# Kernel tuning notes

Hardware: AMD Instinct MI355X
Metric: run time of the kernel (lower is better)

The kernel has to match this reference:

```python
import jax, jax.numpy as jnp
import numpy as np

B, F, HU, HC = 8192, 100, 128, 512


def _lin(key, din, dout, bias=True, scale=0.02):
    k1, k2 = jax.random.split(key)
    w = jax.random.normal(k1, (din, dout), jnp.float32) * scale
    if bias:
        b = jax.random.normal(k2, (dout,), jnp.float32) * scale
        return w, b
    return (w,)


def setup_inputs() -> dict:
    key = jax.random.key(0)
    ks = jax.random.split(key, 24)
    d = {}
    d['feature_list'] = jax.random.normal(ks[0], (B, F), jnp.float32)
    d['is_treat'] = jax.random.uniform(ks[1], (B,), jnp.float32)
    d['emb'] = jax.random.normal(ks[2], (F, HU), jnp.float32) * 0.02
    d['t_w'], d['t_b'] = _lin(ks[3], 1, HU)
    d['qw'], d['qb'] = _lin(ks[4], HU, HU)
    d['kw'], d['kb'] = _lin(ks[5], HU, HU)
    d['vw'], d['vb'] = _lin(ks[6], HU, HU)
    (d['a1w'],) = _lin(ks[7], HU, HU, bias=False)
    d['a2w'], d['a2b'] = _lin(ks[8], HU, HU)
    (d['a3w'],) = _lin(ks[9], HU, 1, bias=False)
    d['c1w'], d['c1b'] = _lin(ks[10], F * HU, HC)
    d['c2w'], d['c2b'] = _lin(ks[11], HC, HC)
    d['c3w'], d['c3b'] = _lin(ks[12], HC, HC // 2)
    d['c4w'], d['c4b'] = _lin(ks[13], HC // 2, HC // 4)
    d['c5w'], d['c5b'] = _lin(ks[14], HC // 4, HC // 8)
    d['clw'], d['clb'] = _lin(ks[15], HC // 8, 1)
    d['ctw'], d['ctb'] = _lin(ks[16], HC // 8, 1)
    d['u1w'], d['u1b'] = _lin(ks[17], HU, HU)
    d['u2w'], d['u2b'] = _lin(ks[18], HU, HU // 2)
    d['u3w'], d['u3b'] = _lin(ks[19], HU // 2, HU // 4)
    d['u4w'], d['u4b'] = _lin(ks[20], HU // 4, HU // 8)
    d['tlw'], d['tlb'] = _lin(ks[21], HU // 8, 1)
    d['utw'], d['utb'] = _lin(ks[22], HU // 8, 1)
    return d


def reference(feature_list, is_treat, emb, t_w, t_b, qw, qb, kw, kb, vw, vb,
              a1w, a2w, a2b, a3w, c1w, c1b, c2w, c2b, c3w, c3b, c4w, c4b,
              c5w, c5b, clw, clb, ctw, ctb, u1w, u1b, u2w, u2b, u3w, u3b,
              u4w, u4b, tlw, tlb, utw, utb):
    elu = jax.nn.elu
    sig = jax.nn.sigmoid
    b, f = feature_list.shape
    h = emb.shape[1]
    # per-feature embedding: [B, F, H]
    x_rep = feature_list[:, :, None] * emb[None, :, :]
    # normalize over the feature axis (dim=1), as in torch.linalg.norm(dim=1)
    nx = x_rep / jnp.linalg.norm(x_rep, axis=1, keepdims=True)
    # self-attention with sigmoid-then-softmax scores
    Q = nx @ qw + qb
    K = nx @ kw + kb
    V = nx @ vw + vb
    scores = jnp.einsum('bfh,bgh->bfg', Q, K) / (h ** 0.5)
    attn_w = jax.nn.softmax(sig(scores), axis=-1)
    xx = jnp.einsum('bfg,bgh->bfh', attn_w, V).reshape(b, f * h)
    # control net tower
    c = elu(xx @ c1w + c1b)
    c = elu(c @ c2w + c2b)
    c = elu(c @ c3w + c3b)
    c = elu(c @ c4w + c4b)
    c = elu(c @ c5w + c5b)  # is_self=True
    c_logit = c @ clw + clb
    c_tau = c @ ctw + ctb
    c_prob = sig(c_logit)
    # treatment representation: Linear(1, hu) on ones -> [B, H]
    t_rep = jnp.ones((b, 1), feature_list.dtype) @ t_w.reshape(1, h) + t_b
    # interaction attention (vectorized over features)
    att = jax.nn.relu(sig(t_rep @ a1w)[:, None, :] + sig(x_rep @ a2w + a2b))
    att = (att @ a3w)[..., 0]  # [B, F]
    attn = jax.nn.softmax(att, axis=1)
    xt = jnp.einsum('bf,bfh->bh', attn, x_rep)
    # uplift net tower
    u = elu(xt @ u1w + u1b)
    u = elu(u @ u2w + u2b)
    u = elu(u @ u3w + u3b)
    u = elu(u @ u4w + u4b)  # is_self=True
    t_logit = u @ tlw + tlb
    u_tau = u @ utw + utb
    t_prob = sig(t_logit)
    return (c_logit, c_prob, c_tau, t_logit, t_prob, u_tau)
```

## Files before the change

kernel.cpp:

```cpp
#include <hip/hip_runtime.h>
#include <hip/hip_bf16.h>

typedef __bf16 bf16;
typedef __bf16 bf16x8 __attribute__((ext_vector_type(8)));
typedef __bf16 bf16x4 __attribute__((ext_vector_type(4)));
typedef float f32x4 __attribute__((ext_vector_type(4)));
typedef unsigned u32x4 __attribute__((ext_vector_type(4)));

#define DEVI static __device__ __forceinline__

DEVI float sigmoidf_(float x){ return 1.0f/(1.0f+__expf(-x)); }
DEVI float eluf_(float x){ return x>0.f ? x : (__expf(x)-1.f); }
DEVI f32x4 mfma16(bf16x8 a, bf16x8 b, f32x4 c){ return __builtin_amdgcn_mfma_f32_16x16x32_bf16(a,b,c,0,0,0); }
DEVI f32x4 mfma8(long a, long b, f32x4 c){ return __builtin_amdgcn_mfma_f32_16x16x32_fp8_fp8(a,b,c,0,0,0); }
DEVI unsigned pack2_(float a, float b){
    union { bf16 v[2]; unsigned u; } t; t.v[0]=(bf16)a; t.v[1]=(bf16)b; return t.u;
}
DEVI unsigned long long pack4_(float a, float b, float c, float d){
    union { bf16 v[4]; unsigned long long u; } t;
    t.v[0]=(bf16)a; t.v[1]=(bf16)b; t.v[2]=(bf16)c; t.v[3]=(bf16)d; return t.u;
}
DEVI unsigned cvtfp8x4_(float a, float b, float c, float d){
    int v = __builtin_amdgcn_cvt_pk_fp8_f32(a, b, 0, false);
    v = __builtin_amdgcn_cvt_pk_fp8_f32(c, d, v, true);
    return (unsigned)v;
}

#define B_ 8192
#define F_ 100
#define FP 112
#define H_ 128
#define KC_ 12800
#define SPLIT_ 4
#define FP8SC 16.0f

#define SWZ(r,bc) ((bc) ^ (((r)&7)<<4))

DEVI void dotrans_(float (*t)[33], const float* in, bf16* out, int R, int C, int bx, int by, int tid){
    int c0 = bx*32, r0 = by*32;
    int tc = tid & 31, tr = tid >> 5;
    #pragma unroll
    for (int i=0;i<4;i++){
        int r = tr + i*8;
        t[r][tc] = in[(size_t)(r0+r)*C + c0 + tc];
    }
    __syncthreads();
    #pragma unroll
    for (int i=0;i<4;i++){
        int ro = tr + i*8;
        out[(size_t)(c0+ro)*R + r0 + tc] = (bf16)t[tc][ro];
    }
}

__global__ void k_prep_all(const float* __restrict__ qw, const float* __restrict__ qb,
                           const float* __restrict__ kw, const float* __restrict__ kb,
                           const float* __restrict__ tw, const float* __restrict__ tb,
                           const float* __restrict__ a1w, const float* __restrict__ vw,
                           const float* __restrict__ a2w, const float* __restrict__ c2w,
                           const float* __restrict__ c3w,
                           bf16* __restrict__ mextT, float* __restrict__ sigt, float* __restrict__ cconst,
                           bf16* __restrict__ wvT, bf16* __restrict__ wa2t,
                           bf16* __restrict__ c2wt, bf16* __restrict__ c3wt){
    __shared__ float t[32][33];
    const float rsc = 0.08838834764831845f;
    int blk = blockIdx.x, tid = threadIdx.x;
    if (blk < 9){
        #pragma unroll 1
        for (int e=0; e<8; ++e){
            int idx = e*256 + tid;
            int n = blk*16 + (idx>>7), h = idx&127;
            float acc = 0.f;
            if (n < 128){
                for (int d=0; d<128; ++d) acc += qw[h*128+d]*kw[n*128+d];
            } else if (n == 128){
                for (int d=0; d<128; ++d) acc += qw[h*128+d]*kb[d];
            } else if (n == 129){
                for (int d=0; d<128; ++d) acc += kw[h*128+d]*qb[d];
            }
            mextT[n*128+h] = (bf16)(acc*rsc);
        }
    } else if (blk == 9){
        if (tid < 128){
            float acc = 0.f;
            for (int h=0; h<128; ++h) acc += (tw[h]+tb[h]) * a1w[h*128+tid];
            sigt[tid] = sigmoidf_(acc);
        } else if (tid == 128){
            float acc = 0.f;
            for (int d=0; d<128; ++d) acc += qb[d]*kb[d];
            cconst[0] = acc*rsc;
        }
    } else if (blk < 26){
        int i = blk-10; dotrans_(t, vw, wvT, 128,128, i&3, i>>2, tid);
    } else if (blk < 42){
        int i = blk-26; dotrans_(t, a2w, wa2t, 128,128, i&3, i>>2, tid);
    } else if (blk < 298){
        int i = blk-42; dotrans_(t, c2w, c2wt, 512,512, i&15, i>>4, tid);
    } else {
        int i = blk-298; dotrans_(t, c3w, c3wt, 512,256, i&7, i>>3, tid);
    }
}

DEVI int kappa_(int k){
    int f = k>>7, h = k&127;
    if (f < 96)
        return (((f>>4)<<3) | (h>>4))*256 + ((f&15)>>2)*64 + (h&15)*4 + (f&3);
    else
        return 12288 + (h>>4)*64 + (h&15)*4 + (f&3);
}

__global__ __launch_bounds__(256,2) void k_gk(
    const float* __restrict__ c1w, unsigned char* __restrict__ c1wtk8,
    const float* __restrict__ feat, const float* __restrict__ emb,
    const bf16* __restrict__ wa2t, const float* __restrict__ a2b,
    const float* __restrict__ a3w, const float* __restrict__ sigt,
    float* __restrict__ attg)
{
    __shared__ char A[37888];
    int blk = blockIdx.x, tid = threadIdx.x;
    if (blk < 6400){
        float (*t)[33] = (float(*)[33])A;
        const int C = 512;
        int c0 = (blk&15)*32, r0 = (blk>>4)*32;
        int tc = tid & 31, tr = tid >> 5;
        #pragma unroll
        for (int i=0;i<4;i++){
            int r = tr + i*8;
            t[r][tc] = c1w[(size_t)(r0+r)*C + c0 + tc];
        }
        __syncthreads();
        #pragma unroll
        for (int i=0;i<4;i++){
            int ro = tr + i*8;
            float x = t[tc][ro]*FP8SC;
            int v = __builtin_amdgcn_cvt_pk_fp8_f32(x, x, 0, false);
            c1wtk8[(size_t)(c0+ro)*KC_ + kappa_(r0+tc)] = (unsigned char)v;
        }
        return;
    }
    bf16 (*sAt)[72] = (bf16(*)[72])A;
    bf16 (*sBt)[72] = (bf16(*)[72])(A + 18432);
    float (*sRed)[128] = (float(*)[128])(A + 36864);
    int w=tid>>6, lane=tid&63, l15=lane&15, l4=lane>>4;
    int m0 = (blk-6400)*128;
    int wr = w>>1, wc = w&1;
    f32x4 acc[4][4];
    #pragma unroll
    for(int mi=0;mi<4;mi++)
        #pragma unroll
        for(int ni=0;ni<4;ni++) acc[mi][ni] = (f32x4){0.f,0.f,0.f,0.f};

    #pragma unroll 1
    for (int k0=0; k0<128; k0+=64){
        __syncthreads();
        #pragma unroll
        for (int t4=0; t4<4; t4++){
            int t = tid + t4*256;
            int row=t>>3, col=(t&7)*8;
            int gr = m0+row;
            int bb = gr/112, ff = gr - bb*112;
            bf16x8 o;
            if (ff < F_){
                float fv = feat[(size_t)bb*F_ + ff];
                const float* ep = emb + ff*H_ + k0 + col;
                f32x4 e0 = *(const f32x4*)ep;
                f32x4 e1 = *(const f32x4*)(ep+4);
                o[0]=(bf16)(fv*e0[0]); o[1]=(bf16)(fv*e0[1]); o[2]=(bf16)(fv*e0[2]); o[3]=(bf16)(fv*e0[3]);
                o[4]=(bf16)(fv*e1[0]); o[5]=(bf16)(fv*e1[1]); o[6]=(bf16)(fv*e1[2]); o[7]=(bf16)(fv*e1[3]);
            } else {
                #pragma unroll
                for (int e=0;e<8;e++) o[e]=(bf16)0.f;
            }
            *(bf16x8*)&sAt[row][col] = o;
            *(bf16x8*)&sBt[row][col] = *(const bf16x8*)(wa2t + row*H_ + k0 + col);
        }
        __syncthreads();
        #pragma unroll
        for(int ks=0;ks<2;ks++){
            bf16x8 af[4], bfr[4];
            #pragma unroll
            for(int mi=0;mi<4;mi++) af[mi] = *(const bf16x8*)&sAt[wr*64+mi*16+l15][ks*32+l4*8];
            #pragma unroll
            for(int ni=0;ni<4;ni++) bfr[ni] = *(const bf16x8*)&sBt[wc*64+ni*16+l15][ks*32+l4*8];
            #pragma unroll
            for(int mi=0;mi<4;mi++)
                #pragma unroll
                for(int ni=0;ni<4;ni++)
                    acc[mi][ni] = mfma16(af[mi], bfr[ni], acc[mi][ni]);
        }
    }
    float sg[4], ab[4], a3[4];
    #pragma unroll
    for (int ni=0;ni<4;ni++){
        int n = wc*64 + ni*16 + l15;
        sg[ni]=sigt[n]; ab[ni]=a2b[n]; a3[ni]=a3w[n];
    }
    #pragma unroll
    for (int mi=0;mi<4;mi++){
        float sj[4] = {0.f,0.f,0.f,0.f};
        #pragma unroll
        for (int ni=0;ni<4;ni++){
            #pragma unroll
            for (int j=0;j<4;j++){
                float u = sigmoidf_(acc[mi][ni][j] + ab[ni]);
                float t = sg[ni] + u;
                t = t>0.f ? t : 0.f;
                sj[j] += t*a3[ni];
            }
        }
        #pragma unroll
        for (int j=0;j<4;j++){
            float v = sj[j];
            #pragma unroll
            for (int m=1;m<16;m<<=1) v += __shfl_xor(v,m,16);
            sj[j]=v;
        }
        if (l15==0){
            #pragma unroll
            for (int j=0;j<4;j++) sRed[wc][wr*64+mi*16+l4*4+j] = sj[j];
        }
    }
    __syncthreads();
    if (tid < 128) attg[(size_t)m0 + tid] = sRed[0][tid] + sRed[1][tid];
}

__global__ __launch_bounds__(512,2) void k_attn2(
    const float* __restrict__ feat, const float* __restrict__ emb,
    const bf16* __restrict__ mextT, const bf16* __restrict__ wvT,
    const float* __restrict__ vb, const float* __restrict__ cconst,
    const float* __restrict__ attg,
    unsigned char* __restrict__ xxb, bf16* __restrict__ xtb)
{
    __shared__ char L[81792];
    char* Lm = L;
    char* Ln = L + 32768;
    float* sFeat  = (float*)(L+61440);
    float* normP  = (float*)(L+62336);
    float* sAw    = (float*)(L+77568);
    float* sNorm  = (float*)(L+79872);
    float* sAlpha = (float*)(L+80384);
    float* sBeta  = (float*)(L+80832);
    float* sInv   = (float*)(L+81280);

    int b = blockIdx.x;
    int tid = threadIdx.x, w = tid>>6, lane = tid&63;
    int l15 = lane&15, l4 = lane>>4;
    bf16 (*sP)[72] = (bf16(*)[72])(L + 61440 + w*2304);

    bf16x8 awv[4];
    #pragma unroll
    for (int kc=0;kc<4;kc++)
        awv[kc] = *(const bf16x8*)(wvT + (w*16+l15)*H_ + kc*32 + l4*8);
    float vbr = vb[w*16+l15];

    #pragma unroll 2
    for (int v = tid; v < 128*16; v += 512){
        int n = v >> 4, cg = (v & 15) * 8;
        *(u32x4*)(Lm + n*256 + SWZ(n, cg*2)) = *(const u32x4*)(mextT + n*128 + cg);
    }
    if (tid < FP) sFeat[tid] = (tid<F_) ? feat[(size_t)b*F_+tid] : 0.f;
    if (w==0){
        const float* ag = attg + (size_t)b*FP;
        float a0 = (lane<F_)? ag[lane] : -1e30f;
        float a1 = (lane+64<F_)? ag[lane+64] : -1e30f;
        float m = fmaxf(a0,a1);
        #pragma unroll
        for(int s=1;s<64;s<<=1) m = fmaxf(m, __shfl_xor(m,s,64));
        float e0 = (lane<F_)? __expf(a0-m):0.f;
        float e1 = (lane+64<F_)? __expf(a1-m):0.f;
        float s = e0+e1;
        #pragma unroll
        for(int t=1;t<64;t<<=1) s += __shfl_xor(s,t,64);
        float inv = 1.f/s;
        if (lane<FP) sAw[lane] = e0*inv;
        if (lane+64<FP) sAw[lane+64] = e1*inv;
    }
    __syncthreads();

    int hp = (tid&63)*2, gg = tid>>6;
    {
        float fa0=0.f, fa1=0.f;
        #pragma unroll 4
        for (int it=0; it<13; ++it){
            int f = gg + 8*it;
            if (f < F_){
                float2 e2 = *(const float2*)(emb + f*H_ + hp);
                float v0 = sFeat[f]*e2.x, v1 = sFeat[f]*e2.y;
                fa0 += v0*v0; fa1 += v1*v1;
            }
        }
        *(float2*)(normP + gg*128 + hp) = make_float2(fa0, fa1);
    }
    __syncthreads();
    if (tid < 128){
        float s = 0.f;
        #pragma unroll
        for (int g2=0; g2<8; ++g2) s += normP[g2*128 + tid];
        sNorm[tid] = sqrtf(s);
    }
    __syncthreads();

    {
        float rn0 = __builtin_amdgcn_rcpf(sNorm[hp]);
        float rn1 = __builtin_amdgcn_rcpf(sNorm[hp+1]);
        #pragma unroll 4
        for (int it=0; it<13; ++it){
            int f = gg + 8*it;
            if (f < F_){
                float2 e2 = *(const float2*)(emb + f*H_ + hp);
                *(unsigned*)(Ln + f*256 + SWZ(f, hp*2)) = pack2_(sFeat[f]*e2.x*rn0, sFeat[f]*e2.y*rn1);
            }
        }
        for (int z=tid; z<768; z+=512){
            int f = 100 + (z>>6), hz = (z&63)*2;
            *(unsigned*)(Ln + f*256 + SWZ(f, hz*2)) = 0u;
        }
    }
    __syncthreads();

    int mt = w;

    if (mt < 7){
        bf16x8 bfr8[4];
        #pragma unroll
        for (int kc=0;kc<4;kc++)
            bfr8[kc] = *(const bf16x8*)(mextT + (128+(l15&1))*H_ + kc*32 + l4*8);
        f32x4 acc = {0.f,0.f,0.f,0.f};
        #pragma unroll
        for (int kc=0;kc<4;kc++){
            bf16x8 a = *(const bf16x8*)(Ln + (mt*16+l15)*256 + SWZ(mt*16+l15, (kc*32+l4*8)*2));
            acc = mfma16(a, bfr8[kc], acc);
        }
        if (l15==0){
            #pragma unroll
            for (int j=0;j<4;j++) sAlpha[mt*16+l4*4+j] = acc[j];
        }
        if (l15==1){
            #pragma unroll
            for (int j=0;j<4;j++) sBeta[mt*16+l4*4+j] = acc[j];
        }
    }
    __syncthreads();

    const float cc = cconst[0];
    unsigned long long uexB[3];
    if (mt < 7){
        bf16x8 afxi[4];
        #pragma unroll
        for (int kc=0;kc<4;kc++)
            afxi[kc] = *(const bf16x8*)(Ln + (mt*16+l15)*256 + SWZ(mt*16+l15, (kc*32+l4*8)*2));
        f32x4 sc[7];
        #pragma unroll
        for (int gt=0; gt<7; gt++) sc[gt] = (f32x4){0.f,0.f,0.f,0.f};
        #pragma unroll
        for (int p=0; p<2; p++){
            #pragma unroll
            for (int nt4=0; nt4<4; nt4++){
                int nt = p*4 + nt4;
                bf16x8 bw[4];
                #pragma unroll
                for (int kc=0;kc<4;kc++)
                    bw[kc] = *(const bf16x8*)(Lm + (nt*16+l15)*256 + SWZ(nt*16+l15, (kc*32+l4*8)*2));
                f32x4 d = {0.f,0.f,0.f,0.f};
                #pragma unroll
                for (int kc=0;kc<4;kc++) d = mfma16(bw[kc], afxi[kc], d);
                *(unsigned long long*)(&sP[l15][nt4*16 + l4*4]) = pack4_(d[0],d[1],d[2],d[3]);
            }
            bf16x8 afs0 = *(const bf16x8*)&sP[l15][l4*8];
            bf16x8 afs1 = *(const bf16x8*)&sP[l15][32+l4*8];
            #pragma unroll
            for (int gt=0; gt<7; gt++){
                int r = gt*16+l15;
                bf16x8 b0 = *(const bf16x8*)(Ln + r*256 + SWZ(r, (p*64 + l4*8)*2));
                bf16x8 b1 = *(const bf16x8*)(Ln + r*256 + SWZ(r, (p*64 + 32 + l4*8)*2));
                sc[gt] = mfma16(b0, afs0, sc[gt]);
                sc[gt] = mfma16(b1, afs1, sc[gt]);
            }
        }
        float aj = sAlpha[mt*16+l15];
        float rs = 0.f;
        #pragma unroll
        for (int gt=0; gt<7; gt++){
            f32x4 bt4 = *(const f32x4*)&sBeta[gt*16+l4*4];
            float e[4];
            #pragma unroll
            for (int j=0;j<4;j++){
                int g = gt*16 + l4*4 + j;
                float val = sc[gt][j] + aj + bt4[j] + cc;
                e[j] = (g<F_) ? __expf(sigmoidf_(val)) : 0.f;
                rs += e[j];
            }
            if (gt < 4)
                *(unsigned long long*)(&sP[l15][gt*16 + l4*4]) = pack4_(e[0],e[1],e[2],e[3]);
            else
                uexB[gt-4] = pack4_(e[0],e[1],e[2],e[3]);
        }
        rs += __shfl_xor(rs, 16, 64);
        rs += __shfl_xor(rs, 32, 64);
        if (l4 == 0) sInv[w*16 + l15] = 1.f/rs;
    } else {
        int h = lane;
        float a0=0.f, a1=0.f;
        #pragma unroll 4
        for (int f=0; f<F_; ++f){
            float awf = sAw[f];
            a0 += awf * (float)*(const bf16*)(Ln + f*256 + SWZ(f, h*2));
            a1 += awf * (float)*(const bf16*)(Ln + f*256 + SWZ(f, (h+64)*2));
        }
        xtb[(size_t)b*H_ + h]      = (bf16)(a0 * sNorm[h]);
        xtb[(size_t)b*H_ + h + 64] = (bf16)(a1 * sNorm[h+64]);
    }

    unsigned long long vpku[7];
    #pragma unroll
    for (int gt=0; gt<7; gt++){
        f32x4 acc = {0.f,0.f,0.f,0.f};
        #pragma unroll
        for (int kc=0;kc<4;kc++){
            int r = gt*16+l15;
            bf16x8 a = *(const bf16x8*)(Ln + r*256 + SWZ(r, (kc*32+l4*8)*2));
            acc = mfma16(a, awv[kc], acc);
        }
        vpku[gt] = pack4_(acc[0]+vbr, acc[1]+vbr, acc[2]+vbr, acc[3]+vbr);
    }
    __syncthreads();

    {
        int hrow = w*16 + l15;
        #pragma unroll
        for (int gt=0; gt<7; gt++)
            *(unsigned long long*)(Lm + hrow*256 + SWZ(hrow, gt*32 + l4*8)) = vpku[gt];
    }
    __syncthreads();

    if (mt < 7){
        bf16x8 ap0 = *(const bf16x8*)&sP[l15][l4*8];
        bf16x8 ap1 = *(const bf16x8*)&sP[l15][32+l4*8];
        f32x4 acc8[8];
        #pragma unroll
        for (int ht=0;ht<8;ht++) acc8[ht] = (f32x4){0.f,0.f,0.f,0.f};
        #pragma unroll
        for (int ht=0; ht<8; ht++){
            int r = ht*16+l15;
            bf16x8 bv0 = *(const bf16x8*)(Lm + r*256 + SWZ(r, (l4*8)*2));
            bf16x8 bv1 = *(const bf16x8*)(Lm + r*256 + SWZ(r, (32+l4*8)*2));
            acc8[ht] = mfma16(ap0, bv0, acc8[ht]);
            acc8[ht] = mfma16(ap1, bv1, acc8[ht]);
        }
        #pragma unroll
        for (int gt=4; gt<7; gt++)
            *(unsigned long long*)(&sP[l15][(gt-4)*16 + l4*4]) = uexB[gt-4];
        *(unsigned long long*)(&sP[l15][48 + l4*4]) = 0ull;
        bf16x8 ap2 = *(const bf16x8*)&sP[l15][l4*8];
        bf16x8 ap3 = *(const bf16x8*)&sP[l15][32+l4*8];
        #pragma unroll
        for (int ht=0; ht<8; ht++){
            int r = ht*16+l15;
            int c2 = 64+l4*8;
            int c3 = 96+l4*8;  if (c3 >= 112) c3 = 96;
            bf16x8 bv2 = *(const bf16x8*)(Lm + r*256 + SWZ(r, c2*2));
            bf16x8 bv3 = *(const bf16x8*)(Lm + r*256 + SWZ(r, c3*2));
            acc8[ht] = mfma16(ap2, bv2, acc8[ht]);
            acc8[ht] = mfma16(ap3, bv3, acc8[ht]);
        }
        float fs[4];
        #pragma unroll
        for (int j=0;j<4;j++) fs[j] = sInv[w*16 + l4*4 + j] * FP8SC;
        #pragma unroll
        for (int ht=0; ht<8; ht++){
            unsigned u = cvtfp8x4_(acc8[ht][0]*fs[0], acc8[ht][1]*fs[1], acc8[ht][2]*fs[2], acc8[ht][3]*fs[3]);
            if (mt < 6){
                *(unsigned*)(xxb + (size_t)b*KC_ + (mt*8+ht)*256 + lane*4) = u;
            } else if (l4 == 0){
                *(unsigned*)(xxb + (size_t)b*KC_ + 12288 + ht*64 + l15*4) = u;
            }
        }
    }
}

__global__ __launch_bounds__(256,2) void k_gemm_fp8(const unsigned char* __restrict__ A,
        const unsigned char* __restrict__ Bt, float* __restrict__ part, int M, int N, int K, int KS)
{
    __shared__ unsigned char sA[128][144];
    __shared__ unsigned char sB[128][144];
    int tid=threadIdx.x, w=tid>>6, lane=tid&63, l15=lane&15, l4=lane>>4;
    int m0 = blockIdx.y*128, n0 = blockIdx.x*128;
    int kbeg = blockIdx.z*KS, kend = kbeg + KS;
    int wr = w>>1, wc = w&1;
    f32x4 acc[4][4];
    #pragma unroll
    for(int mi=0;mi<4;mi++)
        #pragma unroll
        for(int ni=0;ni<4;ni++) acc[mi][ni] = (f32x4){0.f,0.f,0.f,0.f};

    for (int k0=kbeg; k0<kend; k0+=128){
        __syncthreads();
        #pragma unroll
        for (int t8=0;t8<4;t8++){
            int t = tid + t8*256;
            int row=t>>3, col=(t&7)*16;
            *(u32x4*)&sA[row][col] = *(const u32x4*)(A + (size_t)(m0+row)*K + k0 + col);
            *(u32x4*)&sB[row][col] = *(const u32x4*)(Bt + (size_t)(n0+row)*K + k0 + col);
        }
        __syncthreads();
        #pragma unroll
        for(int ks=0;ks<4;ks++){
            long af[4], bfr[4];
            #pragma unroll
            for(int mi=0;mi<4;mi++) af[mi] = *(const long*)&sA[wr*64+mi*16+l15][ks*32+l4*8];
            #pragma unroll
            for(int ni=0;ni<4;ni++) bfr[ni] = *(const long*)&sB[wc*64+ni*16+l15][ks*32+l4*8];
            #pragma unroll
            for(int mi=0;mi<4;mi++)
                #pragma unroll
                for(int ni=0;ni<4;ni++)
                    acc[mi][ni] = mfma8(af[mi], bfr[ni], acc[mi][ni]);
        }
    }
    float* pz = part + (size_t)blockIdx.z*M*N;
    #pragma unroll
    for(int mi=0;mi<4;mi++)
        #pragma unroll
        for(int ni=0;ni<4;ni++){
            int col = n0 + wc*64 + ni*16 + l15;
            #pragma unroll
            for(int j=0;j<4;j++){
                int row = m0 + wr*64 + mi*16 + l4*4 + j;
                pz[(size_t)row*N + col] = acc[mi][ni][j];
            }
        }
}

__global__ void k_c1fin(const float* __restrict__ part, const float* __restrict__ bias,
                        bf16* __restrict__ out){
    const size_t MN = (size_t)B_*512;
    size_t e0 = ((size_t)blockIdx.x*256 + threadIdx.x)*4;
    f32x4 s = *(const f32x4*)(part + e0);
    s += *(const f32x4*)(part + MN + e0);
    s += *(const f32x4*)(part + 2*MN + e0);
    s += *(const f32x4*)(part + 3*MN + e0);
    f32x4 bb = *(const f32x4*)(bias + (e0 & 511));
    const float ds = 1.0f/(FP8SC*FP8SC);
    unsigned long long u = pack4_(eluf_(s[0]*ds+bb[0]), eluf_(s[1]*ds+bb[1]),
                                  eluf_(s[2]*ds+bb[2]), eluf_(s[3]*ds+bb[3]));
    *(unsigned long long*)(out + e0) = u;
}

template<int BN, bool ELU>
__global__ __launch_bounds__(256,2) void k_gemm(const bf16* __restrict__ A, const bf16* __restrict__ Bt,
        const float* __restrict__ bias, bf16* __restrict__ out, int M, int N, int K)
{
    __shared__ bf16 sAt[128][72];
    __shared__ bf16 sBt[BN][72];
    int tid=threadIdx.x, w=tid>>6, lane=tid&63, l15=lane&15, l4=lane>>4;
    int m0 = blockIdx.y*128, n0 = blockIdx.x*BN;
    constexpr int MI = (BN==128)?4:2;
    constexpr int NI = (BN==128)?4:BN/16;
    int wr = (BN==128)? (w>>1) : w;
    int wc = (BN==128)? (w&1) : 0;
    f32x4 acc[MI][NI];
    #pragma unroll
    for(int mi=0;mi<MI;mi++)
        #pragma unroll
        for(int ni=0;ni<NI;ni++) acc[mi][ni] = (f32x4){0.f,0.f,0.f,0.f};

    for (int k0=0; k0<K; k0+=64){
        __syncthreads();
        for (int t=tid; t<128*8; t+=256){
            int row=t>>3, col=(t&7)*8;
            *(bf16x8*)&sAt[row][col] = *(const bf16x8*)(A + (size_t)(m0+row)*K + k0 + col);
        }
        for (int t=tid; t<BN*8; t+=256){
            int row=t>>3, col=(t&7)*8;
            *(bf16x8*)&sBt[row][col] = *(const bf16x8*)(Bt + (size_t)(n0+row)*K + k0 + col);
        }
        __syncthreads();
        #pragma unroll
        for(int ks=0;ks<2;ks++){
            bf16x8 af[MI], bfr[NI];
            #pragma unroll
            for(int mi=0;mi<MI;mi++) af[mi] = *(const bf16x8*)&sAt[wr*(MI*16)+mi*16+l15][ks*32+l4*8];
            #pragma unroll
            for(int ni=0;ni<NI;ni++) bfr[ni] = *(const bf16x8*)&sBt[wc*64+ni*16+l15][ks*32+l4*8];
            #pragma unroll
            for(int mi=0;mi<MI;mi++)
                #pragma unroll
                for(int ni=0;ni<NI;ni++)
                    acc[mi][ni] = mfma16(af[mi], bfr[ni], acc[mi][ni]);
        }
    }
    #pragma unroll
    for(int mi=0;mi<MI;mi++)
        #pragma unroll
        for(int ni=0;ni<NI;ni++){
            int col = n0 + wc*64 + ni*16 + l15;
            float bc = bias[col];
            #pragma unroll
            for(int j=0;j<4;j++){
                int row = m0 + wr*(MI*16) + mi*16 + l4*4 + j;
                float v = acc[mi][ni][j] + bc;
                if (ELU) v = eluf_(v);
                out[(size_t)row*N + col] = (bf16)v;
            }
        }
}

__global__ __launch_bounds__(256,2) void k_tails(const bf16* __restrict__ c3o,
    const float* __restrict__ c4w, const float* __restrict__ c4b,
    const float* __restrict__ c5w, const float* __restrict__ c5b,
    const float* __restrict__ clw, const float* __restrict__ clb,
    const float* __restrict__ ctw, const float* __restrict__ ctb,
    const bf16* __restrict__ xtb,
    const float* __restrict__ u1w, const float* __restrict__ u1b,
    const float* __restrict__ u2w, const float* __restrict__ u2b,
    const float* __restrict__ u3w, const float* __restrict__ u3b,
    const float* __restrict__ u4w, const float* __restrict__ u4b,
    const float* __restrict__ tlw, const float* __restrict__ tlb,
    const float* __restrict__ utw, const float* __restrict__ utb, float* __restrict__ outp)
{
    __shared__ char A[58880];
    int tid = threadIdx.x, blk = blockIdx.x;
    int r0 = (blk>>1)*32;
    if ((blk & 1) == 0){
        float (*sA)[260] = (float(*)[260])A;
        float (*sB)[132] = (float(*)[132])(A + 33280);
        float (*sC)[68]  = (float(*)[68])(A + 50176);
        for (int v=tid; v<32*64; v+=256){
            int r=v>>6, c=(v&63)*4;
            bf16x4 x = *(const bf16x4*)(c3o + (size_t)(r0+r)*256 + c);
            sA[r][c]=(float)x[0]; sA[r][c+1]=(float)x[1]; sA[r][c+2]=(float)x[2]; sA[r][c+3]=(float)x[3];
        }
        __syncthreads();
        {
            int j = tid&127, rb = tid>>7;
            float acc[16];
            #pragma unroll
            for (int i=0;i<16;i++) acc[i]=c4b[j];
            #pragma unroll 4
            for (int h=0;h<256;h++){
                float wv = c4w[h*128+j];
                #pragma unroll
                for (int i=0;i<16;i++) acc[i] += sA[2*i+rb][h]*wv;
            }
            #pragma unroll
            for (int i=0;i<16;i++) sB[2*i+rb][j] = eluf_(acc[i]);
        }
        __syncthreads();
        {
            int j = tid&63, rb = tid>>6;
            float acc[8];
            #pragma unroll
            for (int i=0;i<8;i++) acc[i]=c5b[j];
            #pragma unroll 4
            for (int h=0;h<128;h++){
                float wv = c5w[h*64+j];
                #pragma unroll
                for (int i=0;i<8;i++) acc[i] += sB[4*i+rb][h]*wv;
            }
            #pragma unroll
            for (int i=0;i<8;i++) sC[4*i+rb][j] = eluf_(acc[i]);
        }
        __syncthreads();
        if (tid < 32){
            float r1 = clb[0], r2 = ctb[0];
            #pragma unroll 8
            for (int k=0;k<64;k++){ float v = sC[tid][k]; r1 += v*clw[k]; r2 += v*ctw[k]; }
            int row = r0 + tid;
            outp[row] = r1;
            outp[B_ + row] = sigmoidf_(r1);
            outp[(size_t)2*B_ + row] = r2;
        }
    } else {
        float (*sA)[132] = (float(*)[132])A;
        float (*sB)[132] = (float(*)[132])(A + 16896);
        float (*sC)[68]  = (float(*)[68])(A + 33792);
        float (*sD)[36]  = (float(*)[36])(A + 42496);
        float (*sE)[20]  = (float(*)[20])(A + 47104);
        for (int v=tid; v<32*32; v+=256){
            int r=v>>5, c=(v&31)*4;
            bf16x4 x = *(const bf16x4*)(xtb + (size_t)(r0+r)*128 + c);
            sA[r][c]=(float)x[0]; sA[r][c+1]=(float)x[1]; sA[r][c+2]=(float)x[2]; sA[r][c+3]=(float)x[3];
        }
        __syncthreads();
        {
            int j = tid&127, rb = tid>>7;
            float acc[16];
            #pragma unroll
            for (int i=0;i<16;i++) acc[i]=u1b[j];
            #pragma unroll 4
            for (int h=0;h<128;h++){
                float wv = u1w[h*128+j];
                #pragma unroll
                for (int i=0;i<16;i++) acc[i] += sA[2*i+rb][h]*wv;
            }
            #pragma unroll
            for (int i=0;i<16;i++) sB[2*i+rb][j] = eluf_(acc[i]);
        }
        __syncthreads();
        {
            int j = tid&63, rb = tid>>6;
            float acc[8];
            #pragma unroll
            for (int i=0;i<8;i++) acc[i]=u2b[j];
            #pragma unroll 4
            for (int h=0;h<128;h++){
                float wv = u2w[h*64+j];
                #pragma unroll
                for (int i=0;i<8;i++) acc[i] += sB[4*i+rb][h]*wv;
            }
            #pragma unroll
            for (int i=0;i<8;i++) sC[4*i+rb][j] = eluf_(acc[i]);
        }
        __syncthreads();
        {
            int j = tid&31, rb = tid>>5;
            float acc[4];
            #pragma unroll
            for (int i=0;i<4;i++) acc[i]=u3b[j];
            #pragma unroll 4
            for (int h=0;h<64;h++){
                float wv = u3w[h*32+j];
                #pragma unroll
                for (int i=0;i<4;i++) acc[i] += sC[8*i+rb][h]*wv;
            }
            #pragma unroll
            for (int i=0;i<4;i++) sD[8*i+rb][j] = eluf_(acc[i]);
        }
        __syncthreads();
        {
            int j = tid&15, rb = tid>>4;
            float acc0=u4b[j], acc1=u4b[j];
            #pragma unroll 4
            for (int h=0;h<32;h++){
                float wv = u4w[h*16+j];
                acc0 += sD[rb][h]*wv;
                acc1 += sD[16+rb][h]*wv;
            }
            sE[rb][j] = eluf_(acc0);
            sE[16+rb][j] = eluf_(acc1);
        }
        __syncthreads();
        if (tid < 32){
            float r1 = tlb[0], r2 = utb[0];
            #pragma unroll
            for (int k=0;k<16;k++){ float v = sE[tid][k]; r1 += v*tlw[k]; r2 += v*utw[k]; }
            int row = r0 + tid;
            outp[(size_t)3*B_ + row] = r1;
            outp[(size_t)4*B_ + row] = sigmoidf_(r1);
            outp[(size_t)5*B_ + row] = r2;
        }
    }
}

extern "C" void kernel_launch(void* const* d_in, const int* in_sizes, int n_in,
                              void* d_out, int out_size, void* d_ws, size_t ws_size,
                              hipStream_t stream) {
    const float* feat=(const float*)d_in[0];
    const float* emb =(const float*)d_in[2];
    const float* t_w =(const float*)d_in[3]; const float* t_b=(const float*)d_in[4];
    const float* qw  =(const float*)d_in[5]; const float* qb =(const float*)d_in[6];
    const float* kw  =(const float*)d_in[7]; const float* kb =(const float*)d_in[8];
    const float* vw  =(const float*)d_in[9]; const float* vb =(const float*)d_in[10];
    const float* a1w =(const float*)d_in[11];
    const float* a2w =(const float*)d_in[12]; const float* a2b=(const float*)d_in[13];
    const float* a3w =(const float*)d_in[14];
    const float* c1w =(const float*)d_in[15]; const float* c1b=(const float*)d_in[16];
    const float* c2w =(const float*)d_in[17]; const float* c2b=(const float*)d_in[18];
    const float* c3w =(const float*)d_in[19]; const float* c3b=(const float*)d_in[20];
    const float* c4w =(const float*)d_in[21]; const float* c4b=(const float*)d_in[22];
    const float* c5w =(const float*)d_in[23]; const float* c5b=(const float*)d_in[24];
    const float* clw =(const float*)d_in[25]; const float* clb=(const float*)d_in[26];
    const float* ctw =(const float*)d_in[27]; const float* ctb=(const float*)d_in[28];
    const float* u1w =(const float*)d_in[29]; const float* u1b=(const float*)d_in[30];
    const float* u2w =(const float*)d_in[31]; const float* u2b=(const float*)d_in[32];
    const float* u3w =(const float*)d_in[33]; const float* u3b=(const float*)d_in[34];
    const float* u4w =(const float*)d_in[35]; const float* u4b=(const float*)d_in[36];
    const float* tlw =(const float*)d_in[37]; const float* tlb=(const float*)d_in[38];
    const float* utw =(const float*)d_in[39]; const float* utb=(const float*)d_in[40];
    float* outp = (float*)d_out;

    char* ws = (char*)d_ws;
    size_t off = 0;
    auto alloc = [&](size_t bytes)->char*{ char* p = ws + off; off += (bytes + 255) & ~(size_t)255; return p; };
    unsigned char* xxb = (unsigned char*)alloc((size_t)B_*KC_);
    float* part  = (float*)alloc((size_t)SPLIT_*B_*512*4);
    float* attg  = (float*)alloc((size_t)B_*FP*4);
    bf16* xtb    = (bf16*)alloc((size_t)B_*128*2);
    bf16* cbuf1  = (bf16*)alloc((size_t)B_*512*2);
    bf16* mextT  = (bf16*)alloc(144*128*2);
    bf16* wvT    = (bf16*)alloc(128*128*2);
    bf16* wa2t   = (bf16*)alloc(128*128*2);
    unsigned char* c1wtk8 = (unsigned char*)alloc((size_t)512*KC_);
    bf16* c2wt   = (bf16*)alloc((size_t)512*512*2);
    bf16* c3wt   = (bf16*)alloc((size_t)512*256*2);
    float* sigt  = (float*)alloc(128*4);
    float* cconst= (float*)alloc(4);
    bf16* cbuf2 = (bf16*)(xxb);
    bf16* cbuf3 = (bf16*)(xxb + (16u<<20));
    (void)ws_size; (void)in_sizes; (void)n_in; (void)out_size;

    k_prep_all<<<426,256,0,stream>>>(qw,qb,kw,kb,t_w,t_b,a1w, vw, a2w, c2w, c3w,
                                     mextT, sigt, cconst, wvT, wa2t, c2wt, c3wt);

    k_gk<<<13568,256,0,stream>>>(c1w, c1wtk8, feat, emb, wa2t, a2b, a3w, sigt, attg);

    k_attn2<<<B_,512,0,stream>>>(feat,emb,mextT,wvT,vb,cconst,attg, xxb, xtb);

    k_gemm_fp8<<<dim3(4,64,SPLIT_),256,0,stream>>>(xxb, c1wtk8, part, B_,512,KC_, KC_/SPLIT_);
    k_c1fin<<<4096,256,0,stream>>>(part, c1b, cbuf1);

    k_gemm<128,true><<<dim3(4,64),256,0,stream>>>(cbuf1, c2wt, c2b, cbuf2, B_,512,512);
    k_gemm<64,true><<<dim3(4,64),256,0,stream>>>(cbuf2, c3wt, c3b, cbuf3, B_,256,512);

    k_tails<<<512,256,0,stream>>>(cbuf3,c4w,c4b,c5w,c5b,clw,clb,ctw,ctb,
                                  xtb,u1w,u1b,u2w,u2b,u3w,u3b,u4w,u4b,tlw,tlb,utw,utb,outp);
}
```

Measured before the change: 648.6 us.

## Widen fp8 GEMM tile to 128x256, store bf16 split-K partials, limit attn unroll

```diff
diff --git a/kernel.cpp b/kernel.cpp
--- a/kernel.cpp
+++ b/kernel.cpp
@@ -351,9 +351,9 @@
         f32x4 sc[7];
         #pragma unroll
         for (int gt=0; gt<7; gt++) sc[gt] = (f32x4){0.f,0.f,0.f,0.f};
-        #pragma unroll
+        #pragma unroll 1
         for (int p=0; p<2; p++){
-            #pragma unroll
+            #pragma unroll 2
             for (int nt4=0; nt4<4; nt4++){
                 int nt = p*4 + nt4;
                 bf16x8 bw[4];
@@ -477,15 +477,15 @@
     }
 }
 
-__global__ __launch_bounds__(256,2) void k_gemm_fp8(const unsigned char* __restrict__ A,
-        const unsigned char* __restrict__ Bt, float* __restrict__ part, int M, int N, int K, int KS)
+__global__ __launch_bounds__(512,2) void k_gemm_fp8(const unsigned char* __restrict__ A,
+        const unsigned char* __restrict__ Bt, bf16* __restrict__ part, int M, int N, int K, int KS)
 {
     __shared__ unsigned char sA[128][144];
-    __shared__ unsigned char sB[128][144];
+    __shared__ unsigned char sB[256][144];
     int tid=threadIdx.x, w=tid>>6, lane=tid&63, l15=lane&15, l4=lane>>4;
-    int m0 = blockIdx.y*128, n0 = blockIdx.x*128;
+    int m0 = blockIdx.y*128, n0 = blockIdx.x*256;
     int kbeg = blockIdx.z*KS, kend = kbeg + KS;
-    int wr = w>>1, wc = w&1;
+    int wr = w>>2, wc = w&3;
     f32x4 acc[4][4];
     #pragma unroll
     for(int mi=0;mi<4;mi++)
@@ -495,10 +495,15 @@
     for (int k0=kbeg; k0<kend; k0+=128){
         __syncthreads();
         #pragma unroll
-        for (int t8=0;t8<4;t8++){
-            int t = tid + t8*256;
+        for (int t2=0;t2<2;t2++){
+            int t = tid + t2*512;
             int row=t>>3, col=(t&7)*16;
             *(u32x4*)&sA[row][col] = *(const u32x4*)(A + (size_t)(m0+row)*K + k0 + col);
+        }
+        #pragma unroll
+        for (int t4=0;t4<4;t4++){
+            int t = tid + t4*512;
+            int row=t>>3, col=(t&7)*16;
             *(u32x4*)&sB[row][col] = *(const u32x4*)(Bt + (size_t)(n0+row)*K + k0 + col);
         }
         __syncthreads();
@@ -516,7 +521,7 @@
                     acc[mi][ni] = mfma8(af[mi], bfr[ni], acc[mi][ni]);
         }
     }
-    float* pz = part + (size_t)blockIdx.z*M*N;
+    bf16* pz = part + (size_t)blockIdx.z*M*N;
     #pragma unroll
     for(int mi=0;mi<4;mi++)
         #pragma unroll
@@ -525,23 +530,26 @@
             #pragma unroll
             for(int j=0;j<4;j++){
                 int row = m0 + wr*64 + mi*16 + l4*4 + j;
-                pz[(size_t)row*N + col] = acc[mi][ni][j];
-            }
-        }
-}
-
-__global__ void k_c1fin(const float* __restrict__ part, const float* __restrict__ bias,
+                pz[(size_t)row*N + col] = (bf16)acc[mi][ni][j];
+            }
+        }
+}
+
+__global__ void k_c1fin(const bf16* __restrict__ part, const float* __restrict__ bias,
                         bf16* __restrict__ out){
     const size_t MN = (size_t)B_*512;
     size_t e0 = ((size_t)blockIdx.x*256 + threadIdx.x)*4;
-    f32x4 s = *(const f32x4*)(part + e0);
-    s += *(const f32x4*)(part + MN + e0);
-    s += *(const f32x4*)(part + 2*MN + e0);
-    s += *(const f32x4*)(part + 3*MN + e0);
+    bf16x4 p0 = *(const bf16x4*)(part + e0);
+    bf16x4 p1 = *(const bf16x4*)(part + MN + e0);
+    bf16x4 p2 = *(const bf16x4*)(part + 2*MN + e0);
+    bf16x4 p3 = *(const bf16x4*)(part + 3*MN + e0);
     f32x4 bb = *(const f32x4*)(bias + (e0 & 511));
     const float ds = 1.0f/(FP8SC*FP8SC);
-    unsigned long long u = pack4_(eluf_(s[0]*ds+bb[0]), eluf_(s[1]*ds+bb[1]),
-                                  eluf_(s[2]*ds+bb[2]), eluf_(s[3]*ds+bb[3]));
+    float s0 = ((float)p0[0]+(float)p1[0]+(float)p2[0]+(float)p3[0])*ds + bb[0];
+    float s1 = ((float)p0[1]+(float)p1[1]+(float)p2[1]+(float)p3[1])*ds + bb[1];
+    float s2 = ((float)p0[2]+(float)p1[2]+(float)p2[2]+(float)p3[2])*ds + bb[2];
+    float s3 = ((float)p0[3]+(float)p1[3]+(float)p2[3]+(float)p3[3])*ds + bb[3];
+    unsigned long long u = pack4_(eluf_(s0), eluf_(s1), eluf_(s2), eluf_(s3));
     *(unsigned long long*)(out + e0) = u;
 }
 
@@ -782,7 +790,7 @@
     size_t off = 0;
     auto alloc = [&](size_t bytes)->char*{ char* p = ws + off; off += (bytes + 255) & ~(size_t)255; return p; };
     unsigned char* xxb = (unsigned char*)alloc((size_t)B_*KC_);
-    float* part  = (float*)alloc((size_t)SPLIT_*B_*512*4);
+    bf16* part   = (bf16*)alloc((size_t)SPLIT_*B_*512*2);
     float* attg  = (float*)alloc((size_t)B_*FP*4);
     bf16* xtb    = (bf16*)alloc((size_t)B_*128*2);
     bf16* cbuf1  = (bf16*)alloc((size_t)B_*512*2);
@@ -805,7 +813,7 @@
 
     k_attn2<<<B_,512,0,stream>>>(feat,emb,mextT,wvT,vb,cconst,attg, xxb, xtb);
 
-    k_gemm_fp8<<<dim3(4,64,SPLIT_),256,0,stream>>>(xxb, c1wtk8, part, B_,512,KC_, KC_/SPLIT_);
+    k_gemm_fp8<<<dim3(2,64,SPLIT_),512,0,stream>>>(xxb, c1wtk8, part, B_,512,KC_, KC_/SPLIT_);
     k_c1fin<<<4096,256,0,stream>>>(part, c1b, cbuf1);
 
     k_gemm<128,true><<<dim3(4,64),256,0,stream>>>(cbuf1, c2wt, c2b, cbuf2, B_,512,512);
```

New measurement: 632.2 us, median of 2. 2.5% less time.
